# Optimization experiments

Hardware: AMD Instinct MI355X
Metric: run time of the kernel (lower is better)

Reference implementation:

```python
import jax, jax.numpy as jnp
import numpy as np

B, N, D, F = 32, 4096, 256, 256

def setup_inputs() -> dict:
    key = jax.random.key(0)
    k1, k2, k3, k4 = jax.random.split(key, 4)
    raw_input = jax.random.normal(k1, (B, N, D), dtype=jnp.float32)
    input_plus_attention = jax.random.normal(k2, (B, F), dtype=jnp.float32)
    W = jax.random.normal(k3, (F, N), dtype=jnp.float32) * 0.02
    b = jnp.zeros((N,), dtype=jnp.float32)
    # keras 'uniform' initializer: U(-0.05, 0.05)
    threshold = jax.random.uniform(k4, (1,), minval=-0.05, maxval=0.05, dtype=jnp.float32)
    return {"raw_input": raw_input, "input_plus_attention": input_plus_attention,
            "W": W, "b": b, "threshold": threshold}

def reference(raw_input, input_plus_attention, W, b, threshold):
    # Dense(units, relu): [B,F] @ [F,N] -> [B,N]
    x = jax.nn.relu(input_plus_attention @ W + b)
    # BinaryLayer: 1.0 where x > threshold else 0.0 -> row selection mask [B,N]
    mask = x > threshold[0]
    # TF boolean_mask + reshape(B,-1,D) performs per-batch stream compaction of
    # selected rows. JAX needs static shapes, so compact selected rows to the
    # front (stable order preserved) and zero-pad the tail to length N.
    order = jnp.argsort(jnp.where(mask, 0, 1).astype(jnp.int32), axis=1)  # stable: selected first
    gathered = jnp.take_along_axis(raw_input, order[:, :, None], axis=1)  # [B,N,D]
    counts = jnp.sum(mask, axis=1, keepdims=True)                          # [B,1]
    keep = jnp.arange(N)[None, :] < counts                                 # [B,N]
    out = jnp.where(keep[:, :, None], gathered, jnp.zeros((), raw_input.dtype))
    return out
```

## Files before the change

### kernel.cpp

```cpp
#include <hip/hip_runtime.h>
#include <hip/hip_bf16.h>
#include <stdint.h>


#define BB 32
#define NN 4096
#define DD 256
#define FF 256
#define COLS 16
#define CH (NN / COLS)
#define ASTRIDE (FF + 4)

typedef float f4 __attribute__((ext_vector_type(4)));

__global__ __launch_bounds__(256) void mask_kernel(
    const float* __restrict__ A,
    const float* __restrict__ W,
    const float* __restrict__ bias,
    const float* __restrict__ thr_p,
    uint16_t* __restrict__ bits)
{
    __shared__ float a_sh[BB * ASTRIDE];
    __shared__ float wT[COLS * ASTRIDE];

    const int t     = threadIdx.x;
    const int chunk = blockIdx.x;
    const int n0    = chunk * COLS;

    for (int i = t; i < BB * FF; i += 256) {
        int b = i >> 8, f = i & 255;
        a_sh[b * ASTRIDE + f] = A[i];
    }
    for (int i = t; i < FF * COLS; i += 256) {
        int f = i >> 4, c = i & 15;
        wT[c * ASTRIDE + f] = W[(size_t)f * NN + n0 + c];
    }
    __syncthreads();

    const float thr = thr_p[0];
    const int c  = t & 15;
    const int b1 = t >> 4;
    const int b2 = b1 + 16;

    const f4* a1p = reinterpret_cast<const f4*>(a_sh + b1 * ASTRIDE);
    const f4* a2p = reinterpret_cast<const f4*>(a_sh + b2 * ASTRIDE);
    const f4* wp  = reinterpret_cast<const f4*>(wT   + c  * ASTRIDE);

    double s0 = 0.0, s1 = 0.0, s2 = 0.0, s3 = 0.0;
    #pragma unroll 8
    for (int fs = 0; fs < FF / 4; ++fs) {
        f4 w4 = wp[fs];
        f4 a1 = a1p[fs];
        f4 a2 = a2p[fs];
        s0 = fma((double)a1.x, (double)w4.x, s0);
        s0 = fma((double)a1.y, (double)w4.y, s0);
        s1 = fma((double)a1.z, (double)w4.z, s1);
        s1 = fma((double)a1.w, (double)w4.w, s1);
        s2 = fma((double)a2.x, (double)w4.x, s2);
        s2 = fma((double)a2.y, (double)w4.y, s2);
        s3 = fma((double)a2.z, (double)w4.z, s3);
        s3 = fma((double)a2.w, (double)w4.w, s3);
    }
    const float bi = bias[n0 + c];
    const float v1 = (float)(s0 + s1) + bi;
    const float v2 = (float)(s2 + s3) + bi;
    const int m1 = (fmaxf(v1, 0.f) > thr) ? 1 : 0;
    const int m2 = (fmaxf(v2, 0.f) > thr) ? 1 : 0;

    unsigned long long bal1 = __ballot(m1);
    unsigned long long bal2 = __ballot(m2);
    if (c == 0) {
        const int g = (t & 63) >> 4;
        bits[b1 * CH + chunk] = (uint16_t)((bal1 >> (16 * g)) & 0xFFFF);
        bits[b2 * CH + chunk] = (uint16_t)((bal2 >> (16 * g)) & 0xFFFF);
    }
}

__global__ __launch_bounds__(256) void scan_kernel(
    const uint16_t* __restrict__ bits,
    int* __restrict__ order,
    int* __restrict__ count)
{
    const int b = blockIdx.x;
    const int t = threadIdx.x;
    __shared__ int wsum[4];

    unsigned m = bits[b * CH + t];
    const int s = __popc(m);

    const int lane = t & 63;
    const int wid  = t >> 6;
    int incl = s;
    #pragma unroll
    for (int d = 1; d < 64; d <<= 1) {
        int x = __shfl_up(incl, d, 64);
        if (lane >= d) incl += x;
    }
    if (lane == 63) wsum[wid] = incl;
    __syncthreads();
    if (t == 0) {
        int run = 0;
        #pragma unroll
        for (int i = 0; i < 4; ++i) { int x = wsum[i]; wsum[i] = run; run += x; }
        count[b] = run;
    }
    __syncthreads();

    int base = wsum[wid] + (incl - s);
    int* ob = order + (size_t)b * NN + base;
    const int n0 = t * COLS;
    while (m) {
        *ob++ = n0 + (__ffs(m) - 1);
        m &= m - 1;
    }
}

__global__ __launch_bounds__(256) void gather_kernel(
    const float* __restrict__ raw,
    const int* __restrict__ order,
    const int* __restrict__ count,
    float* __restrict__ out)
{
    const int b    = blockIdx.y;
    const int wid  = threadIdx.x >> 6;
    const int lane = threadIdx.x & 63;
    const int j0   = blockIdx.x * 8 + wid * 2;

    const int cnt = count[b];
    const int* ob = order + (size_t)b * NN;
    const f4* rawp = reinterpret_cast<const f4*>(raw);
    f4* outp = reinterpret_cast<f4*>(out);

    f4 r0 = {0.f, 0.f, 0.f, 0.f};
    f4 r1 = {0.f, 0.f, 0.f, 0.f};
    if (j0 < cnt) {
        const int src = ob[j0];
        r0 = __builtin_nontemporal_load(rawp + ((size_t)b * NN + src) * (DD / 4) + lane);
    }
    if (j0 + 1 < cnt) {
        const int src = ob[j0 + 1];
        r1 = __builtin_nontemporal_load(rawp + ((size_t)b * NN + src) * (DD / 4) + lane);
    }
    __builtin_nontemporal_store(r0, outp + ((size_t)b * NN + j0)     * (DD / 4) + lane);
    __builtin_nontemporal_store(r1, outp + ((size_t)b * NN + j0 + 1) * (DD / 4) + lane);
}

extern "C" void kernel_launch(void* const* d_in, const int* in_sizes, int n_in,
                              void* d_out, int out_size, void* d_ws, size_t ws_size,
                              hipStream_t stream) {
    const float* raw  = (const float*)d_in[0];
    const float* A    = (const float*)d_in[1];
    const float* W    = (const float*)d_in[2];
    const float* bias = (const float*)d_in[3];
    const float* thr  = (const float*)d_in[4];
    float* out = (float*)d_out;

    uint16_t* bits  = (uint16_t*)d_ws;
    int*      order = (int*)((char*)d_ws + 65536);
    int*      count = order + (size_t)BB * NN;

    mask_kernel<<<CH, 256, 0, stream>>>(A, W, bias, thr, bits);
    scan_kernel<<<BB, 256, 0, stream>>>(bits, order, count);
    gather_kernel<<<dim3(NN / 8, BB), 256, 0, stream>>>(raw, order, count, out);
}
```

Measured before the change: 60.08 us.

## Fuse scan into gather kernel by recomputing per-batch prefix sums per block

Removes the separate scan kernel and the global order/count buffers. Each gather block re-reads the batch's 256 mask words, does a block prefix scan, and writes only the source indices for its 8 output rows into shared memory. This saves one kernel launch and the order array round trip through global memory. In exchange, the scan is repeated redundantly in every one of the 512 blocks per batch and adds two barriers before the gather loads.

```diff
diff --git a/kernel.cpp b/kernel.cpp
--- a/kernel.cpp
+++ b/kernel.cpp
@@ -10,6 +10,7 @@
 #define COLS 16
 #define CH (NN / COLS)
 #define ASTRIDE (FF + 4)
+#define ROWS_PER_BLK 8
 
 typedef float f4 __attribute__((ext_vector_type(4)));
 
@@ -76,14 +77,18 @@
     }
 }
 
-__global__ __launch_bounds__(256) void scan_kernel(
+__global__ __launch_bounds__(256) void gather_kernel(
+    const float* __restrict__ raw,
     const uint16_t* __restrict__ bits,
-    int* __restrict__ order,
-    int* __restrict__ count)
+    float* __restrict__ out)
 {
-    const int b = blockIdx.x;
-    const int t = threadIdx.x;
+    const int b   = blockIdx.y;
+    const int t   = threadIdx.x;
+    const int j0b = blockIdx.x * ROWS_PER_BLK;
+
     __shared__ int wsum[4];
+    __shared__ int cnt_sh;
+    __shared__ int order_sh[ROWS_PER_BLK];
 
     unsigned m = bits[b * CH + t];
     const int s = __popc(m);
@@ -102,43 +107,37 @@
         int run = 0;
         #pragma unroll
         for (int i = 0; i < 4; ++i) { int x = wsum[i]; wsum[i] = run; run += x; }
-        count[b] = run;
+        cnt_sh = run;
     }
     __syncthreads();
 
     int base = wsum[wid] + (incl - s);
-    int* ob = order + (size_t)b * NN + base;
-    const int n0 = t * COLS;
-    while (m) {
-        *ob++ = n0 + (__ffs(m) - 1);
-        m &= m - 1;
+    if (base < j0b + ROWS_PER_BLK && base + s > j0b) {
+        const int n0 = t * COLS;
+        while (m) {
+            const int pos = __ffs(m) - 1;
+            const unsigned rel = (unsigned)(base - j0b);
+            if (rel < ROWS_PER_BLK) order_sh[rel] = n0 + pos;
+            ++base;
+            if (base >= j0b + ROWS_PER_BLK) break;
+            m &= m - 1;
+        }
     }
-}
+    __syncthreads();
 
-__global__ __launch_bounds__(256) void gather_kernel(
-    const float* __restrict__ raw,
-    const int* __restrict__ order,
-    const int* __restrict__ count,
-    float* __restrict__ out)
-{
-    const int b    = blockIdx.y;
-    const int wid  = threadIdx.x >> 6;
-    const int lane = threadIdx.x & 63;
-    const int j0   = blockIdx.x * 8 + wid * 2;
-
-    const int cnt = count[b];
-    const int* ob = order + (size_t)b * NN;
+    const int cnt = cnt_sh;
     const f4* rawp = reinterpret_cast<const f4*>(raw);
     f4* outp = reinterpret_cast<f4*>(out);
+    const int j0 = j0b + wid * 2;
 
     f4 r0 = {0.f, 0.f, 0.f, 0.f};
     f4 r1 = {0.f, 0.f, 0.f, 0.f};
     if (j0 < cnt) {
-        const int src = ob[j0];
+        const int src = order_sh[j0 - j0b];
         r0 = __builtin_nontemporal_load(rawp + ((size_t)b * NN + src) * (DD / 4) + lane);
     }
     if (j0 + 1 < cnt) {
-        const int src = ob[j0 + 1];
+        const int src = order_sh[j0 + 1 - j0b];
         r1 = __builtin_nontemporal_load(rawp + ((size_t)b * NN + src) * (DD / 4) + lane);
     }
     __builtin_nontemporal_store(r0, outp + ((size_t)b * NN + j0)     * (DD / 4) + lane);
@@ -155,11 +154,8 @@
     const float* thr  = (const float*)d_in[4];
     float* out = (float*)d_out;
 
-    uint16_t* bits  = (uint16_t*)d_ws;
-    int*      order = (int*)((char*)d_ws + 65536);
-    int*      count = order + (size_t)BB * NN;
+    uint16_t* bits = (uint16_t*)d_ws;
 
     mask_kernel<<<CH, 256, 0, stream>>>(A, W, bias, thr, bits);
-    scan_kernel<<<BB, 256, 0, stream>>>(bits, order, count);
-    gather_kernel<<<dim3(NN / 8, BB), 256, 0, stream>>>(raw, order, count, out);
+    gather_kernel<<<dim3(NN / ROWS_PER_BLK, BB), 256, 0, stream>>>(raw, bits, out);
 }
```

After: 61.45 us. +2.3%, slower.
